# Kernel optimization log

Hardware: AMD Instinct MI355X
Metric: run time of the kernel (lower is better)

The kernel has to match this reference:

```python
import jax, jax.numpy as jnp
import numpy as np

MINI_BLOCK = 4

def setup_inputs() -> dict:
    key = jax.random.key(0)
    k1, k2 = jax.random.split(key)
    B, IN, OUT = 4096, 4096, 4096
    gy, gx = OUT // MINI_BLOCK, IN // MINI_BLOCK
    x = jax.random.normal(k1, (B, IN), dtype=jnp.float32)
    eigens = jax.random.normal(k2, (gy, gx, MINI_BLOCK), dtype=jnp.float32)
    return {"x": x, "eigens": eigens}

def reference(x, eigens):
    # Block-circulant linear: out[b, y, :] = sum_x circconv(eigens[y, x], x_blk[b, x])
    # computed in the frequency domain. Original code used two-sided rfft +
    # complex_mult + irfft per (b, y, x) block and summed over x; since the FFT
    # and complex product are linear, we contract over x in frequency space
    # with an einsum instead of materializing the (B, gy, gx, block) tensor.
    gy, gx, blk = eigens.shape
    xb = x.reshape(-1, gx, blk)                      # (B, gx, blk)
    f_eig = jnp.fft.rfft(eigens, axis=-1)            # (gy, gx, blk//2+1) complex
    f_x = jnp.fft.rfft(xb, axis=-1)                  # (B, gx, blk//2+1)
    f_out = jnp.einsum('yxk,bxk->byk', f_eig, f_x)   # contract over gx
    out = jnp.fft.irfft(f_out, n=blk, axis=-1)       # (B, gy, blk)
    return out.reshape(-1, gy * blk)
```

## Files before the change

kernel.cpp:

```cpp
#include <hip/hip_runtime.h>


typedef __attribute__((ext_vector_type(8))) short bf16x8_t;
typedef __attribute__((ext_vector_type(4))) float f32x4_t;
typedef __attribute__((ext_vector_type(8))) unsigned short u16x8;

#define NDIM 4096
#define TILE 128
#define BK 32

__device__ __forceinline__ unsigned short f2bf(float f) {
    unsigned int u = __builtin_bit_cast(unsigned int, f);
    u += 0x7fffu + ((u >> 16) & 1u);
    return (unsigned short)(u >> 16);
}

__device__ __forceinline__ void async_copy16(const void* g, void* l) {
    __builtin_amdgcn_global_load_lds(
        (const __attribute__((address_space(1))) void*)g,
        (__attribute__((address_space(3))) void*)l,
        16, 0, 0);
}

__global__ __launch_bounds__(256) void fwd_x_kernel(const float* __restrict__ x,
                                                    unsigned short* __restrict__ xp) {
    int gid = blockIdx.x * 256 + threadIdx.x;
    int b   = gid >> 7;
    int j0  = (gid & 127) * 8;
    const float4* src = (const float4*)(x + (size_t)b * NDIM + j0 * 4);
    u16x8 s0, sr, si, s2;
#pragma unroll
    for (int i = 0; i < 8; ++i) {
        float4 v = src[i];
        s0[i] = f2bf(v.x + v.y + v.z + v.w);
        sr[i] = f2bf(v.x - v.z);
        si[i] = f2bf(v.w - v.y);
        s2[i] = f2bf(v.x - v.y + v.z - v.w);
    }
    unsigned short* dst = xp + (size_t)b * NDIM + j0;
    *(u16x8*)(dst + 0)    = s0;
    *(u16x8*)(dst + 1024) = sr;
    *(u16x8*)(dst + 2048) = si;
    *(u16x8*)(dst + 3072) = s2;
}

__global__ __launch_bounds__(256) void build_b_kernel(const float* __restrict__ eig,
                                                      unsigned short* __restrict__ B) {
    int gid = blockIdx.x * 256 + threadIdx.x;
    int y   = gid >> 7;
    int x0  = (gid & 127) * 8;
    const float4* src = (const float4*)(eig + ((size_t)y * 1024 + x0) * 4);
    u16x8 e0, er, ei, nei, e2;
#pragma unroll
    for (int i = 0; i < 8; ++i) {
        float4 v = src[i];
        e0[i]  = f2bf(v.x + v.y + v.z + v.w);
        float r = v.x - v.z, s = v.w - v.y;
        er[i]  = f2bf(r);
        ei[i]  = f2bf(s);
        nei[i] = f2bf(-s);
        e2[i]  = f2bf(v.x - v.y + v.z - v.w);
    }
    *(u16x8*)(B + (size_t)y * 1024 + x0) = e0;
    unsigned short* b1r = B + 1048576 + (size_t)y * 2048;
    *(u16x8*)(b1r + x0)        = er;
    *(u16x8*)(b1r + 1024 + x0) = nei;
    unsigned short* b1i = B + 3145728 + (size_t)y * 2048;
    *(u16x8*)(b1i + x0)        = ei;
    *(u16x8*)(b1i + 1024 + x0) = er;
    *(u16x8*)(B + 5242880 + (size_t)y * 1024 + x0) = e2;
}

__global__ __launch_bounds__(256, 2) void gemm_seg_kernel(
        const unsigned short* __restrict__ A,
        const unsigned short* __restrict__ B,
        float* __restrict__ C) {
    __shared__ unsigned short lA[TILE * BK];
    __shared__ unsigned short lB[TILE * BK];

    const int Ks[4]   = {1024, 2048, 2048, 1024};
    const int Aoff[4] = {0, 1024, 1024, 3072};
    const size_t Boff[4] = {0u, 1048576u, 3145728u, 5242880u};

    const int seg  = blockIdx.x >> 3;
    const int nseg = blockIdx.x & 7;
    const int K    = Ks[seg];
    const int aoff = Aoff[seg];
    const unsigned short* Bs = B + Boff[seg];

    const int t    = threadIdx.x;
    const int lane = t & 63;
    const int w    = t >> 6;
    const int wm   = (w >> 1) * 64;
    const int wn   = (w & 1) * 64;
    const int lr   = lane & 15;
    const int quad = lane >> 4;

    const int blkM = blockIdx.y;

    const int e0 = t * 8;
    const int r0 = e0 >> 5;
    const int c0 = e0 & 31;

    const unsigned short* pa0 = A + (size_t)(blkM * TILE + r0) * NDIM + aoff + c0;
    const unsigned short* pa1 = pa0 + (size_t)64 * NDIM;
    const unsigned short* pb0 = Bs + (size_t)(nseg * TILE + r0) * K + c0;
    const unsigned short* pb1 = pb0 + (size_t)64 * K;

    unsigned short* dA0 = &lA[e0];
    unsigned short* dA1 = &lA[2048 + e0];
    unsigned short* dB0 = &lB[e0];
    unsigned short* dB1 = &lB[2048 + e0];

    const unsigned short* la0 = &lA[(wm + lr) * BK + quad * 8];
    const unsigned short* lb0 = &lB[(wn + lr) * BK + quad * 8];

    f32x4_t acc[4][4] = {};

    for (int k0 = 0; k0 < K; k0 += BK) {
        async_copy16(pa0 + k0, dA0);
        async_copy16(pa1 + k0, dA1);
        async_copy16(pb0 + k0, dB0);
        async_copy16(pb1 + k0, dB1);
        asm volatile("s_waitcnt vmcnt(0)" ::: "memory");
        __syncthreads();

        bf16x8_t af[4], bfr[4];
#pragma unroll
        for (int i = 0; i < 4; ++i)
            af[i] = *(const bf16x8_t*)(la0 + i * 16 * BK);
#pragma unroll
        for (int i = 0; i < 4; ++i)
            bfr[i] = *(const bf16x8_t*)(lb0 + i * 16 * BK);

#pragma unroll
        for (int mt = 0; mt < 4; ++mt)
#pragma unroll
            for (int nt = 0; nt < 4; ++nt)
                acc[mt][nt] = __builtin_amdgcn_mfma_f32_16x16x32_bf16(
                    af[mt], bfr[nt], acc[mt][nt], 0, 0, 0);

        __syncthreads();
    }

    const int orow0 = blkM * TILE + wm + quad * 4;
    const int ocol0 = seg * 1024 + nseg * TILE + wn + lr;
#pragma unroll
    for (int mt = 0; mt < 4; ++mt) {
#pragma unroll
        for (int r = 0; r < 4; ++r) {
            float* dst = C + (size_t)(orow0 + mt * 16 + r) * NDIM + ocol0;
#pragma unroll
            for (int nt = 0; nt < 4; ++nt)
                dst[nt * 16] = acc[mt][nt][r];
        }
    }
}

__global__ __launch_bounds__(256) void post_kernel(float* __restrict__ O) {
    float* row = O + (size_t)blockIdx.x * NDIM;
    const int t = threadIdx.x;
    float v0[4], vr[4], vi[4], v2[4];
#pragma unroll
    for (int i = 0; i < 4; ++i) {
        int y = t + i * 256;
        v0[i] = row[y];
        vr[i] = row[1024 + y];
        vi[i] = row[2048 + y];
        v2[i] = row[3072 + y];
    }
    __syncthreads();
#pragma unroll
    for (int i = 0; i < 4; ++i) {
        int y = t + i * 256;
        float4 o;
        o.x = 0.25f * (v0[i] + 2.0f * vr[i] + v2[i]);
        o.y = 0.25f * (v0[i] - 2.0f * vi[i] - v2[i]);
        o.z = 0.25f * (v0[i] - 2.0f * vr[i] + v2[i]);
        o.w = 0.25f * (v0[i] + 2.0f * vi[i] - v2[i]);
        *(float4*)&row[4 * y] = o;
    }
}

extern "C" void kernel_launch(void* const* d_in, const int* in_sizes, int n_in,
                              void* d_out, int out_size, void* d_ws, size_t ws_size,
                              hipStream_t stream) {
    const float* x   = (const float*)d_in[0];
    const float* eig = (const float*)d_in[1];
    float* out = (float*)d_out;

    unsigned short* Xp = (unsigned short*)d_ws;
    unsigned short* Bp = Xp + (size_t)NDIM * NDIM;

    fwd_x_kernel<<<(NDIM * 128) / 256, 256, 0, stream>>>(x, Xp);
    build_b_kernel<<<(1024 * 128) / 256, 256, 0, stream>>>(eig, Bp);

    dim3 grid(32, NDIM / TILE);
    gemm_seg_kernel<<<grid, 256, 0, stream>>>(Xp, Bp, out);

    post_kernel<<<NDIM, 256, 0, stream>>>(out);
}
```

Measured before the change: 227.7 us.

## Use Karatsuba 3-mult complex product to split GEMM into five equal K=1024 segments

The complex middle-frequency product is rewritten with a Gauss/Karatsuba three-multiplication form. X gets an extra r+m plane and B is laid out as five K=1024 planes (e0, er, m-r, m+r, e2), so every GEMM segment has the same length instead of two K=2048 segments. The real and imaginary parts are reassembled in the post kernel from an extra workspace buffer. The GEMM occupancy hint rises from 2 to 5 blocks per SM, and a fallback path with remapped block ordering is kept for when the workspace is too small. This trades fewer MFMA FLOPs and balanced blocks for more preprocessing writes, an extra fp32 buffer, and possible bf16 cancellation error in the Karatsuba terms.

Result: no change. 230.9 us (+1.4%).

```diff
diff --git a/kernel.cpp b/kernel.cpp
--- a/kernel.cpp
+++ b/kernel.cpp
@@ -22,8 +22,178 @@
         16, 0, 0);
 }
 
-__global__ __launch_bounds__(256) void fwd_x_kernel(const float* __restrict__ x,
-                                                    unsigned short* __restrict__ xp) {
+
+__global__ __launch_bounds__(256) void fwd_x_k(const float* __restrict__ x,
+                                               unsigned short* __restrict__ xp) {
+    int gid = blockIdx.x * 256 + threadIdx.x;
+    int b   = gid >> 7;
+    int j0  = (gid & 127) * 8;
+    const float4* src = (const float4*)(x + (size_t)b * NDIM + j0 * 4);
+    u16x8 s0, sr, si, ss, s2;
+#pragma unroll
+    for (int i = 0; i < 8; ++i) {
+        float4 v = src[i];
+        float r = v.x - v.z, m = v.w - v.y;
+        s0[i] = f2bf(v.x + v.y + v.z + v.w);
+        sr[i] = f2bf(r);
+        si[i] = f2bf(m);
+        ss[i] = f2bf(r + m);
+        s2[i] = f2bf(v.x - v.y + v.z - v.w);
+    }
+    unsigned short* dst = xp + (size_t)b * 5120 + j0;
+    *(u16x8*)(dst + 0)    = s0;
+    *(u16x8*)(dst + 1024) = sr;
+    *(u16x8*)(dst + 2048) = si;
+    *(u16x8*)(dst + 3072) = ss;
+    *(u16x8*)(dst + 4096) = s2;
+}
+
+__global__ __launch_bounds__(256) void build_b_k(const float* __restrict__ eig,
+                                                 unsigned short* __restrict__ B) {
+    int gid = blockIdx.x * 256 + threadIdx.x;
+    int y   = gid >> 7;
+    int x0  = (gid & 127) * 8;
+    const float4* src = (const float4*)(eig + ((size_t)y * 1024 + x0) * 4);
+    u16x8 e0, er, ed, es, e2;
+#pragma unroll
+    for (int i = 0; i < 8; ++i) {
+        float4 v = src[i];
+        float r = v.x - v.z, m = v.w - v.y;
+        e0[i] = f2bf(v.x + v.y + v.z + v.w);
+        er[i] = f2bf(r);
+        ed[i] = f2bf(m - r);
+        es[i] = f2bf(m + r);
+        e2[i] = f2bf(v.x - v.y + v.z - v.w);
+    }
+    size_t p = (size_t)y * 1024 + x0;
+    *(u16x8*)(B + 0u       + p) = e0;
+    *(u16x8*)(B + 1048576u + p) = er;
+    *(u16x8*)(B + 2097152u + p) = ed;
+    *(u16x8*)(B + 3145728u + p) = es;
+    *(u16x8*)(B + 4194304u + p) = e2;
+}
+
+__global__ __launch_bounds__(256, 5) void gemm_k(
+        const unsigned short* __restrict__ A,
+        const unsigned short* __restrict__ B,
+        float* __restrict__ C,
+        float* __restrict__ K3) {
+    __shared__ unsigned short lA[TILE * BK];
+    __shared__ unsigned short lB[TILE * BK];
+
+    const int aoffs[5] = {0, 3072, 1024, 2048, 4096};
+
+    const int seg  = blockIdx.x >> 3;
+    const int nseg = blockIdx.x & 7;
+    const int blkM = blockIdx.y;
+
+    const int t    = threadIdx.x;
+    const int lane = t & 63;
+    const int w    = t >> 6;
+    const int wm   = (w >> 1) * 64;
+    const int wn   = (w & 1) * 64;
+    const int lr   = lane & 15;
+    const int quad = lane >> 4;
+
+    const int e0 = t * 8;
+    const int r0 = e0 >> 5;
+    const int c0 = e0 & 31;
+
+    const unsigned short* pa0 = A + (size_t)(blkM * TILE + r0) * 5120 + aoffs[seg] + c0;
+    const unsigned short* pa1 = pa0 + (size_t)64 * 5120;
+    const unsigned short* pb0 = B + (size_t)seg * 1048576 +
+                                (size_t)(nseg * TILE + r0) * 1024 + c0;
+    const unsigned short* pb1 = pb0 + (size_t)64 * 1024;
+
+    unsigned short* dA0 = &lA[e0];
+    unsigned short* dA1 = &lA[2048 + e0];
+    unsigned short* dB0 = &lB[e0];
+    unsigned short* dB1 = &lB[2048 + e0];
+
+    const unsigned short* la0 = &lA[(wm + lr) * BK + quad * 8];
+    const unsigned short* lb0 = &lB[(wn + lr) * BK + quad * 8];
+
+    f32x4_t acc[4][4] = {};
+
+    for (int k0 = 0; k0 < 1024; k0 += BK) {
+        async_copy16(pa0 + k0, dA0);
+        async_copy16(pa1 + k0, dA1);
+        async_copy16(pb0 + k0, dB0);
+        async_copy16(pb1 + k0, dB1);
+        asm volatile("s_waitcnt vmcnt(0)" ::: "memory");
+        __syncthreads();
+
+        bf16x8_t af[4], bfr[4];
+#pragma unroll
+        for (int i = 0; i < 4; ++i)
+            af[i] = *(const bf16x8_t*)(la0 + i * 16 * BK);
+#pragma unroll
+        for (int i = 0; i < 4; ++i)
+            bfr[i] = *(const bf16x8_t*)(lb0 + i * 16 * BK);
+
+#pragma unroll
+        for (int mt = 0; mt < 4; ++mt)
+#pragma unroll
+            for (int nt = 0; nt < 4; ++nt)
+                acc[mt][nt] = __builtin_amdgcn_mfma_f32_16x16x32_bf16(
+                    af[mt], bfr[nt], acc[mt][nt], 0, 0, 0);
+
+        __syncthreads();
+    }
+
+    float* dstbase;
+    int    cstride, colbase;
+    if (seg == 3) { dstbase = K3; cstride = 1024; colbase = nseg * TILE; }
+    else {
+        int regio = (seg < 3) ? seg : 3;
+        dstbase = C; cstride = NDIM; colbase = regio * 1024 + nseg * TILE;
+    }
+
+    const int orow0 = blkM * TILE + wm + quad * 4;
+    const int ocol0 = colbase + wn + lr;
+#pragma unroll
+    for (int mt = 0; mt < 4; ++mt) {
+#pragma unroll
+        for (int r = 0; r < 4; ++r) {
+            float* dst = dstbase + (size_t)(orow0 + mt * 16 + r) * cstride + ocol0;
+#pragma unroll
+            for (int nt = 0; nt < 4; ++nt)
+                dst[nt * 16] = acc[mt][nt][r];
+        }
+    }
+}
+
+__global__ __launch_bounds__(256) void post_k(float* __restrict__ O,
+                                              const float* __restrict__ K3) {
+    float* row = O + (size_t)blockIdx.x * NDIM;
+    const float* k3row = K3 + (size_t)blockIdx.x * 1024;
+    const int t = threadIdx.x;
+    float v0[4], vr[4], vi[4], v2[4];
+#pragma unroll
+    for (int i = 0; i < 4; ++i) {
+        int y = t + i * 256;
+        float k1 = row[1024 + y];
+        v0[i] = row[y];
+        vr[i] = k1 - k3row[y];
+        vi[i] = k1 + row[2048 + y];
+        v2[i] = row[3072 + y];
+    }
+    __syncthreads();
+#pragma unroll
+    for (int i = 0; i < 4; ++i) {
+        int y = t + i * 256;
+        float4 o;
+        o.x = 0.25f * (v0[i] + 2.0f * vr[i] + v2[i]);
+        o.y = 0.25f * (v0[i] - 2.0f * vi[i] - v2[i]);
+        o.z = 0.25f * (v0[i] - 2.0f * vr[i] + v2[i]);
+        o.w = 0.25f * (v0[i] + 2.0f * vi[i] - v2[i]);
+        *(float4*)&row[4 * y] = o;
+    }
+}
+
+
+__global__ __launch_bounds__(256) void fwd_x_fb(const float* __restrict__ x,
+                                                unsigned short* __restrict__ xp) {
     int gid = blockIdx.x * 256 + threadIdx.x;
     int b   = gid >> 7;
     int j0  = (gid & 127) * 8;
@@ -44,8 +214,8 @@
     *(u16x8*)(dst + 3072) = s2;
 }
 
-__global__ __launch_bounds__(256) void build_b_kernel(const float* __restrict__ eig,
-                                                      unsigned short* __restrict__ B) {
+__global__ __launch_bounds__(256) void build_b_fb(const float* __restrict__ eig,
+                                                  unsigned short* __restrict__ B) {
     int gid = blockIdx.x * 256 + threadIdx.x;
     int y   = gid >> 7;
     int x0  = (gid & 127) * 8;
@@ -71,7 +241,7 @@
     *(u16x8*)(B + 5242880 + (size_t)y * 1024 + x0) = e2;
 }
 
-__global__ __launch_bounds__(256, 2) void gemm_seg_kernel(
+__global__ __launch_bounds__(256, 2) void gemm_fb(
         const unsigned short* __restrict__ A,
         const unsigned short* __restrict__ B,
         float* __restrict__ C) {
@@ -82,8 +252,11 @@
     const int Aoff[4] = {0, 1024, 1024, 3072};
     const size_t Boff[4] = {0u, 1048576u, 3145728u, 5242880u};
 
-    const int seg  = blockIdx.x >> 3;
-    const int nseg = blockIdx.x & 7;
+    int lin = blockIdx.x;
+    int seg, nseg, blkM;
+    if (lin < 512) { seg = 1 + ((lin >> 3) & 1); nseg = lin & 7; blkM = lin >> 4; }
+    else { int i = lin - 512; seg = ((i >> 3) & 1) * 3; nseg = i & 7; blkM = i >> 4; }
+
     const int K    = Ks[seg];
     const int aoff = Aoff[seg];
     const unsigned short* Bs = B + Boff[seg];
@@ -96,8 +269,6 @@
     const int lr   = lane & 15;
     const int quad = lane >> 4;
 
-    const int blkM = blockIdx.y;
-
     const int e0 = t * 8;
     const int r0 = e0 >> 5;
     const int c0 = e0 & 31;
@@ -157,7 +328,7 @@
     }
 }
 
-__global__ __launch_bounds__(256) void post_kernel(float* __restrict__ O) {
+__global__ __launch_bounds__(256) void post_fb(float* __restrict__ O) {
     float* row = O + (size_t)blockIdx.x * NDIM;
     const int t = threadIdx.x;
     float v0[4], vr[4], vi[4], v2[4];
@@ -182,6 +353,7 @@
     }
 }
 
+
 extern "C" void kernel_launch(void* const* d_in, const int* in_sizes, int n_in,
                               void* d_out, int out_size, void* d_ws, size_t ws_size,
                               hipStream_t stream) {
@@ -189,14 +361,25 @@
     const float* eig = (const float*)d_in[1];
     float* out = (float*)d_out;
 
-    unsigned short* Xp = (unsigned short*)d_ws;
-    unsigned short* Bp = Xp + (size_t)NDIM * NDIM;
-
-    fwd_x_kernel<<<(NDIM * 128) / 256, 256, 0, stream>>>(x, Xp);
-    build_b_kernel<<<(1024 * 128) / 256, 256, 0, stream>>>(eig, Bp);
-
-    dim3 grid(32, NDIM / TILE);
-    gemm_seg_kernel<<<grid, 256, 0, stream>>>(Xp, Bp, out);
-
-    post_kernel<<<NDIM, 256, 0, stream>>>(out);
-}
+    const size_t NEED = (size_t)(40 + 10 + 16) * 1024 * 1024;
+
+    if (ws_size >= NEED) {
+        unsigned short* Xp = (unsigned short*)d_ws;
+        unsigned short* Bp = (unsigned short*)((char*)d_ws + 41943040u);
+        float*          K3 = (float*)((char*)d_ws + 52428800u);
+
+        fwd_x_k<<<(NDIM * 128) / 256, 256, 0, stream>>>(x, Xp);
+        build_b_k<<<(1024 * 128) / 256, 256, 0, stream>>>(eig, Bp);
+        dim3 grid(40, NDIM / TILE);
+        gemm_k<<<grid, 256, 0, stream>>>(Xp, Bp, out, K3);
+        post_k<<<NDIM, 256, 0, stream>>>(out, K3);
+    } else {
+        unsigned short* Xp = (unsigned short*)d_ws;
+        unsigned short* Bp = Xp + (size_t)NDIM * NDIM;
+
+        fwd_x_fb<<<(NDIM * 128) / 256, 256, 0, stream>>>(x, Xp);
+        build_b_fb<<<(1024 * 128) / 256, 256, 0, stream>>>(eig, Bp);
+        gemm_fb<<<dim3(1024, 1), 256, 0, stream>>>(Xp, Bp, out);
+        post_fb<<<NDIM, 256, 0, stream>>>(out);
+    }
+}
```
